# Kernel tuning notes

Measured on AMD Instinct MI355X. Metric: run time of the kernel, lower is better.

Reference implementation:

```python
import jax, jax.numpy as jnp
import numpy as np

N = 4096
D = 256
GW_EPSILON = 0.05
GW_MAX_ITER = 5
SINKHORN_MAX_ITER = 20
GAMMA = 1.0
LOG_EPS = 1e-10


def _sinkhorn(M, p, q, eps, n_iters):
    """Entropic OT: returns transport plan for cost M with marginals p, q."""
    K = jnp.exp(-M / eps)  # [n, n] Gibbs kernel

    def body(i, uv):
        u, v = uv
        u = p / (K @ v)
        v = q / (K.T @ u)
        return (u, v)

    u0 = jnp.ones_like(p)
    v0 = jnp.ones_like(q)
    u, v = jax.lax.fori_loop(0, n_iters, body, (u0, v0))
    return u[:, None] * K * v[None, :]  # diag(u) K diag(v)


def _entropic_gw(C1, C2, p, q, eps, gw_iters, sink_iters):
    """Entropic Gromov-Wasserstein with square_loss (POT-style fixed point)."""
    # square_loss decomposition: f1(a)=a^2, f2(b)=b^2, h1(a)=a, h2(b)=2b
    constC = (C1 ** 2 @ p)[:, None] + (C2 ** 2 @ q)[None, :]  # [n, n]
    hC1 = C1
    hC2 = 2.0 * C2
    T = jnp.outer(p, q)  # init plan

    def gw_body(i, T):
        tens = constC - hC1 @ (T @ hC2.T)  # gradient of GW objective
        return _sinkhorn(tens, p, q, eps, sink_iters)

    return jax.lax.fori_loop(0, gw_iters, gw_body, T)


def setup_inputs() -> dict:
    key = jax.random.key(0)
    k1, k2 = jax.random.split(key)
    features_1 = jax.random.normal(k1, (N, D), dtype=jnp.float32)
    features_2 = jax.random.normal(k2, (N, D), dtype=jnp.float32)
    return {"features_1": features_1, "features_2": features_2}


def reference(features_1, features_2):
    out_1 = features_1 / jnp.linalg.norm(features_1, axis=1, keepdims=True)
    out_2 = features_2 / jnp.linalg.norm(features_2, axis=1, keepdims=True)
    daa = 1.0 - out_1 @ out_1.T  # cosine-distance Gram, [n, n]
    dbb = 1.0 - out_2 @ out_2.T
    daa = daa / jnp.max(daa)
    dbb = dbb / jnp.max(dbb)
    n = daa.shape[0]
    p = jnp.full((n,), 1.0 / n, dtype=daa.dtype)
    q = jnp.full((n,), 1.0 / n, dtype=dbb.dtype)
    gw = _entropic_gw(daa, dbb, p, q, GW_EPSILON, GW_MAX_ITER, SINKHORN_MAX_ITER)
    loss = -jnp.sum(jnp.log(jnp.diag(gw) + LOG_EPS))
    return loss * GAMMA
```

## Files before the change

kernel.cpp:

```cpp
#include <hip/hip_runtime.h>

#define N4K 4096
#define DFEAT 256
constexpr float P_UNIF = 1.0f / 4096.0f;

typedef __attribute__((ext_vector_type(8))) short bf16x8;
typedef __attribute__((ext_vector_type(4))) float f32x4;

__device__ __forceinline__ float bfl(unsigned u) { return __uint_as_float(u << 16); }
__device__ __forceinline__ float bfh(unsigned u) { return __uint_as_float(u & 0xffff0000u); }
__device__ __forceinline__ unsigned short f2bf(float f) {
  unsigned u = __float_as_uint(f);
  u += 0x7fffu + ((u >> 16) & 1u);
  return (unsigned short)(u >> 16);
}
__device__ __forceinline__ unsigned char f2fp8(float v) {
  v = fminf(v, 448.0f);
  if (v < 0.015625f) return (unsigned char)__float2uint_rn(v * 512.0f);
  unsigned u = __float_as_uint(v);
  u += 0x7FFFFu + ((u >> 20) & 1u);
  return (unsigned char)(((u >> 20) & 0x7FF) - 960);
}
__device__ __forceinline__ void load_lds16(const void* g, void* l) {
  __builtin_amdgcn_global_load_lds(
      (const __attribute__((address_space(1))) void*)g,
      (__attribute__((address_space(3))) void*)l, 16, 0, 0);
}

#if __has_builtin(__builtin_amdgcn_cvt_pk_f32_fp8)
#define FP8_HW 1
#else
#define FP8_HW 0
#endif

__global__ void k_normalize(const float* __restrict__ in, unsigned short* __restrict__ out) {
  const int wv = threadIdx.x >> 6, lane = threadIdx.x & 63;
  const int row = blockIdx.x * 4 + wv;
  const float4 v = ((const float4*)(in + (size_t)row * DFEAT))[lane];
  float ss = v.x * v.x + v.y * v.y + v.z * v.z + v.w * v.w;
#pragma unroll
  for (int off = 32; off; off >>= 1) ss += __shfl_xor(ss, off);
  const float inv = rsqrtf(ss);
  unsigned a = (unsigned)f2bf(v.x * inv) | ((unsigned)f2bf(v.y * inv) << 16);
  unsigned b = (unsigned)f2bf(v.z * inv) | ((unsigned)f2bf(v.w * inv) << 16);
  ((uint2*)(out + (size_t)row * DFEAT))[lane] = make_uint2(a, b);
}

__global__ void k_transpose(const unsigned short* __restrict__ in,
                            unsigned short* __restrict__ out, int R, int C) {
  __shared__ unsigned short t[64][65];
  const int tid = threadIdx.x;
  const int tx = tid & 63, ty = tid >> 6;
  const int c0 = blockIdx.x * 64, r0 = blockIdx.y * 64;
#pragma unroll
  for (int k = 0; k < 16; k++) {
    const int r = ty * 16 + k;
    t[r][tx] = in[(size_t)(r0 + r) * C + c0 + tx];
  }
  __syncthreads();
#pragma unroll
  for (int k = 0; k < 16; k++) {
    const int r = ty * 16 + k;
    out[(size_t)(c0 + r) * R + r0 + tx] = t[tx][r];
  }
}

__global__ void k_zerof(float* __restrict__ p, int n) {
  const int i = blockIdx.x * 256 + threadIdx.x;
  if (i < n) p[i] = 0.0f;
}

__global__ __launch_bounds__(256) void k_gemm_bt(
    const unsigned short* __restrict__ A, const unsigned short* __restrict__ B,
    int ld, int kChunk, unsigned short* __restrict__ out, float* __restrict__ outf,
    int ldo, int mode, const float* __restrict__ ctE,
    const float* __restrict__ dm1, const float* __restrict__ dm2,
    float* __restrict__ psum, float* __restrict__ psq, float* __restrict__ dmx,
    unsigned char* __restrict__ K8, const float* __restrict__ shiftp)
{
  __shared__ __align__(16) unsigned char SMEM[16384];
  __shared__ float cs[128], cq[128];
  __shared__ float wmx[4];
  unsigned short* Als = (unsigned short*)SMEM;
  unsigned short* Bls = (unsigned short*)(SMEM + 8192);
  const int tid = threadIdx.x;
  const int w = tid >> 6, lane = tid & 63;
  const int wr = w >> 1, wc = w & 1;
  const int mbase = blockIdx.y * 128, nbase = blockIdx.x * 128;
  const int kBase = blockIdx.z * kChunk;

  if (mode == 4 && tid < 128) { cs[tid] = 0.f; cq[tid] = 0.f; }

  const f32x4 fz = {0.f, 0.f, 0.f, 0.f};
  f32x4 acc[4][4];
#pragma unroll
  for (int m = 0; m < 4; m++)
#pragma unroll
    for (int n = 0; n < 4; n++) acc[m][n] = fz;

  const int sRow = lane >> 2;
  const int sCol = (lane & 3) * 8;
  const unsigned short* gA = A + (size_t)(mbase + w * 32 + sRow) * ld + sCol;
  const unsigned short* gB = B + (size_t)(nbase + w * 32 + sRow) * ld + sCol;
  unsigned short* lA0 = &Als[(w * 2 + 0) * 512];
  unsigned short* lA1 = &Als[(w * 2 + 1) * 512];
  unsigned short* lB0 = &Bls[(w * 2 + 0) * 512];
  unsigned short* lB1 = &Bls[(w * 2 + 1) * 512];

  const int rA = lane & 15, kg = (lane >> 4) * 8;

  for (int k0 = kBase; k0 < kBase + kChunk; k0 += 32) {
    __syncthreads();
    load_lds16(gA + k0, lA0);
    load_lds16(gA + (size_t)16 * ld + k0, lA1);
    load_lds16(gB + k0, lB0);
    load_lds16(gB + (size_t)16 * ld + k0, lB1);
    __syncthreads();
    bf16x8 a[4], b[4];
#pragma unroll
    for (int m = 0; m < 4; m++)
      a[m] = *(const bf16x8*)&Als[(wr * 64 + m * 16 + rA) * 32 + kg];
#pragma unroll
    for (int n = 0; n < 4; n++)
      b[n] = *(const bf16x8*)&Bls[(wc * 64 + n * 16 + rA) * 32 + kg];
#pragma unroll
    for (int m = 0; m < 4; m++)
#pragma unroll
      for (int n = 0; n < 4; n++)
        acc[m][n] = __builtin_amdgcn_mfma_f32_16x16x32_bf16(a[m], b[n], acc[m][n], 0, 0, 0);
  }

  if (mode == 4) {
    float mx = -2.0f;
#pragma unroll
    for (int n = 0; n < 4; n++) {
      float sv = 0.f, sq2 = 0.f;
#pragma unroll
      for (int m = 0; m < 4; m++)
#pragma unroll
        for (int r = 0; r < 4; r++) {
          const float val = acc[m][n][r];
          sv += val; sq2 += val * val;
          mx = fmaxf(mx, -val);
        }
      const int lcol = wc * 64 + n * 16 + (lane & 15);
      atomicAdd(&cs[lcol], sv);
      atomicAdd(&cq[lcol], sq2);
    }
#pragma unroll
    for (int off = 32; off; off >>= 1) mx = fmaxf(mx, __shfl_xor(mx, off));
    if (lane == 0) wmx[w] = mx;
    __syncthreads();
    if (tid == 0)
      atomicMax((int*)dmx, __float_as_int(fmaxf(fmaxf(wmx[0], wmx[1]), fmaxf(wmx[2], wmx[3]))));
    if (tid < 128) {
      atomicAdd(&psum[nbase + tid], cs[tid]);
      atomicAdd(&psq[nbase + tid], cq[tid]);
    }
    return;
  }

  const int lrow16 = (lane >> 4) * 4;
  if (mode == 3) {
    float* ef = (float*)SMEM;
    for (int m = 0; m < 4; m++) {
      __syncthreads();
#pragma unroll
      for (int n = 0; n < 4; n++) {
        const int col = wc * 64 + n * 16 + (lane & 15);
#pragma unroll
        for (int r = 0; r < 4; r++)
          ef[(wr * 16 + lrow16 + r) * 128 + col] = acc[m][n][r];
      }
      __syncthreads();
#pragma unroll
      for (int h = 0; h < 4; h++) {
        const int t = tid + h * 256;
        const int cr = t >> 5, cc = (t & 31) * 4;
        const int grow = mbase + (cr >> 4) * 64 + m * 16 + (cr & 15);
        *(uint4*)&outf[((size_t)blockIdx.z * (gridDim.y * 128) + grow) * ldo + nbase + cc]
            = *(uint4*)&ef[cr * 128 + cc];
      }
    }
  } else if (mode == 2) {
    const float sArg = 40.0f / ((1.0f + *dm1) * (1.0f + *dm2));
    const float sh = *shiftp;
    unsigned short* eb = (unsigned short*)SMEM;
    unsigned char* eb8 = (unsigned char*)(SMEM + 8704);
    for (int m = 0; m < 4; m++) {
      __syncthreads();
#pragma unroll
      for (int n = 0; n < 4; n++) {
        const int col = wc * 64 + n * 16 + (lane & 15);
        const float cv = ctE[nbase + col] + sh;
#pragma unroll
        for (int r = 0; r < 4; r++) {
          const float val = __expf(fmaf(sArg, acc[m][n][r], -cv));
          eb[(wr * 16 + lrow16 + r) * 136 + col] = f2bf(val);
          eb8[(wr * 16 + lrow16 + r) * 144 + col] = f2fp8(val);
        }
      }
      __syncthreads();
#pragma unroll
      for (int h = 0; h < 2; h++) {
        const int t = tid + h * 256;
        const int cr = t >> 4, cc = (t & 15) * 8;
        const int grow = mbase + (cr >> 4) * 64 + m * 16 + (cr & 15);
        *(uint4*)&out[(size_t)grow * ldo + nbase + cc] = *(uint4*)&eb[cr * 136 + cc];
      }
      {
        const int cr = tid >> 3, cc = (tid & 7) * 16;
        const int grow = mbase + (cr >> 4) * 64 + m * 16 + (cr & 15);
        *(uint4*)&K8[(size_t)grow * N4K + nbase + cc] = *(uint4*)&eb8[cr * 144 + cc];
      }
    }
  } else {
    unsigned short* eb = (unsigned short*)SMEM;
    for (int m = 0; m < 4; m++) {
      __syncthreads();
#pragma unroll
      for (int n = 0; n < 4; n++) {
        const int col = wc * 64 + n * 16 + (lane & 15);
#pragma unroll
        for (int r = 0; r < 4; r++)
          eb[(wr * 16 + lrow16 + r) * 136 + col] = f2bf(acc[m][n][r]);
      }
      __syncthreads();
#pragma unroll
      for (int h = 0; h < 2; h++) {
        const int t = tid + h * 256;
        const int cr = t >> 4, cc = (t & 15) * 8;
        const int grow = mbase + (cr >> 4) * 64 + m * 16 + (cr & 15);
        *(uint4*)&out[(size_t)grow * ldo + nbase + cc] = *(uint4*)&eb[cr * 136 + cc];
      }
    }
  }
}

__global__ void k_ctfinal(const float* __restrict__ psum, const float* __restrict__ psq,
                          const float* __restrict__ dm1p, const float* __restrict__ dm2p,
                          float* __restrict__ ctE, float* __restrict__ ctsum) {
  __shared__ float red[256];
  const int tid = threadIdx.x;
  const int j = blockIdx.x * 256 + tid;
  const float g2 = psum[j] * (1.0f / N4K);
  const float s2 = psq[j] * (1.0f / N4K);
  const float m1 = 1.0f + *dm1p, m2 = 1.0f + *dm2p;
  const float v = ((1.0f - 2.0f * g2 + s2) / (m2 * m2) + (2.0f / (m1 * m2)) * g2) * 20.0f;
  ctE[j] = v;
  red[tid] = v;
  __syncthreads();
  for (int st = 128; st > 0; st >>= 1) {
    if (tid < st) red[tid] += red[tid + st];
    __syncthreads();
  }
  if (tid == 0) atomicAdd(ctsum, red[0]);
}

__global__ void k_yt0(const unsigned short* __restrict__ X2t, unsigned short* __restrict__ Yt,
                      float* __restrict__ x2sum) {
  __shared__ float red[256];
  const int d = blockIdx.x, t = threadIdx.x;
  const unsigned short* row = X2t + (size_t)d * N4K;
  const uint4 q = *(const uint4*)&row[t * 16];
  const uint4 q2 = *(const uint4*)&row[t * 16 + 8];
  float s = bfl(q.x) + bfh(q.x) + bfl(q.y) + bfh(q.y) + bfl(q.z) + bfh(q.z)
          + bfl(q.w) + bfh(q.w) + bfl(q2.x) + bfh(q2.x) + bfl(q2.y) + bfh(q2.y)
          + bfl(q2.z) + bfh(q2.z) + bfl(q2.w) + bfh(q2.w);
  red[t] = s;
  __syncthreads();
  for (int st = 128; st > 0; st >>= 1) {
    if (t < st) red[t] += red[t + st];
    __syncthreads();
  }
  if (t == 0) x2sum[d] = red[0];
  const unsigned short pv = f2bf(red[0] * (P_UNIF * P_UNIF));
  const unsigned pk = (unsigned)pv | ((unsigned)pv << 16);
  uint4* dst = (uint4*)(Yt + (size_t)d * N4K);
  dst[t] = make_uint4(pk, pk, pk, pk);
  dst[t + 256] = make_uint4(pk, pk, pk, pk);
}

__global__ void k_x2v(const unsigned short* __restrict__ X2t, const float* __restrict__ v,
                      unsigned short* __restrict__ X2vt) {
  const int d = blockIdx.x, t = threadIdx.x;
  const int i0 = t * 16;
  const unsigned short* src = X2t + (size_t)d * N4K + i0;
  unsigned short* dst = X2vt + (size_t)d * N4K + i0;
  const uint4 a = *(const uint4*)src;
  const uint4 b = *(const uint4*)(src + 8);
  const float4 v0 = *(const float4*)&v[i0];
  const float4 v1 = *(const float4*)&v[i0 + 4];
  const float4 v2 = *(const float4*)&v[i0 + 8];
  const float4 v3 = *(const float4*)&v[i0 + 12];
  unsigned r0 = (unsigned)f2bf(bfl(a.x) * v0.x) | ((unsigned)f2bf(bfh(a.x) * v0.y) << 16);
  unsigned r1 = (unsigned)f2bf(bfl(a.y) * v0.z) | ((unsigned)f2bf(bfh(a.y) * v0.w) << 16);
  unsigned r2 = (unsigned)f2bf(bfl(a.z) * v1.x) | ((unsigned)f2bf(bfh(a.z) * v1.y) << 16);
  unsigned r3 = (unsigned)f2bf(bfl(a.w) * v1.z) | ((unsigned)f2bf(bfh(a.w) * v1.w) << 16);
  unsigned r4 = (unsigned)f2bf(bfl(b.x) * v2.x) | ((unsigned)f2bf(bfh(b.x) * v2.y) << 16);
  unsigned r5 = (unsigned)f2bf(bfl(b.y) * v2.z) | ((unsigned)f2bf(bfh(b.y) * v2.w) << 16);
  unsigned r6 = (unsigned)f2bf(bfl(b.z) * v3.x) | ((unsigned)f2bf(bfh(b.z) * v3.y) << 16);
  unsigned r7 = (unsigned)f2bf(bfl(b.w) * v3.z) | ((unsigned)f2bf(bfh(b.w) * v3.w) << 16);
  *(uint4*)dst = make_uint4(r0, r1, r2, r3);
  *(uint4*)(dst + 8) = make_uint4(r4, r5, r6, r7);
}

__global__ void k_redY(const float* __restrict__ Yp, const float* __restrict__ u,
                       unsigned short* __restrict__ Yt) {
  __shared__ float t[64][65];
  const int tid = threadIdx.x;
  const int tx = tid & 63, ty = tid >> 6;
  const int r0 = blockIdx.x * 64, c0 = blockIdx.y * 64;
#pragma unroll
  for (int k = 0; k < 16; k++) {
    const int r = ty * 16 + k;
    const size_t off = (size_t)(r0 + r) * 256 + c0 + tx;
    float s = 0.f;
#pragma unroll
    for (int z = 0; z < 4; z++) s += Yp[(size_t)z * (N4K * 256) + off];
    t[r][tx] = s;
  }
  __syncthreads();
  const float uu = u[r0 + tx];
#pragma unroll
  for (int k = 0; k < 16; k++) {
    const int r = ty * 16 + k;
    Yt[(size_t)(c0 + r) * N4K + r0 + tx] = f2bf(t[tx][r] * uu);
  }
}

__global__ void k_redPT(const float* __restrict__ Pp, unsigned short* __restrict__ PTb) {
  const int idx = blockIdx.x * 256 + threadIdx.x;
  float s = 0.f;
#pragma unroll
  for (int z = 0; z < 16; z++) s += Pp[z * 65536 + idx];
  PTb[idx] = f2bf(s);
}

__global__ void k_zcol(const unsigned short* __restrict__ Zb, float* __restrict__ zpart) {
  const int c = threadIdx.x;
  const int r0 = blockIdx.x * 64;
  float s = 0.f;
  for (int r = 0; r < 64; r++)
    s += bfl((unsigned)Zb[(size_t)(r0 + r) * 256 + c]);
  zpart[blockIdx.x * 256 + c] = s;
}

__global__ void k_shift(const float* __restrict__ zpart, const float* __restrict__ x2sum,
                        const float* __restrict__ ctsum, const float* __restrict__ dm1,
                        const float* __restrict__ dm2, float* __restrict__ shift) {
  __shared__ float red[256];
  const int c = threadIdx.x;
  float zc = 0.f;
#pragma unroll
  for (int b = 0; b < 64; b++) zc += zpart[b * 256 + c];
  red[c] = zc * x2sum[c];
  __syncthreads();
  for (int st = 128; st > 0; st >>= 1) {
    if (c < st) red[c] += red[c + st];
    __syncthreads();
  }
  if (c == 0) {
    const float meanacc = red[0] * (1.0f / (16777216.0f));
    const float sArg = 40.0f / ((1.0f + *dm1) * (1.0f + *dm2));
    shift[0] = sArg * meanacc - ctsum[0] * (1.0f / N4K);
  }
}

__global__ __launch_bounds__(512) void k_sink8(
    const unsigned char* __restrict__ K8, const float* __restrict__ vin,
    float* __restrict__ u, float* __restrict__ partials, int first, int last)
{
  __shared__ float vs[N4K];
  __shared__ float lut[256];
  __shared__ float us[16];
  const int tid = threadIdx.x;
  if (tid < 256) {
    const int e = (tid >> 3) & 15, m = tid & 7;
    lut[tid] = e ? ldexpf((float)(8 + m), e - 10) : ldexpf((float)m, -9);
  }
  if (first) {
    for (int i = tid; i < N4K; i += 512) vs[i] = 1.0f;
  } else {
    float4* vl = (float4*)vs;
    const float4* vg = (const float4*)vin;
    vl[tid] = vg[tid];
    vl[tid + 512] = vg[tid + 512];
  }
  __syncthreads();
  const int wv = tid >> 6, lane = tid & 63;
  const int row0 = blockIdx.x * 16;

#if FP8_HW
#define DEC4(W, J, ACC) { \
    auto _lo = __builtin_amdgcn_cvt_pk_f32_fp8((int)(W), false); \
    auto _hi = __builtin_amdgcn_cvt_pk_f32_fp8((int)(W), true);  \
    ACC += _lo[0] * vs[(J)] + _lo[1] * vs[(J) + 1] + _hi[0] * vs[(J) + 2] + _hi[1] * vs[(J) + 3]; }
#else
#define DEC4(W, J, ACC) { \
    ACC += lut[(W) & 255] * vs[(J)] + lut[((W) >> 8) & 255] * vs[(J) + 1] \
         + lut[((W) >> 16) & 255] * vs[(J) + 2] + lut[(W) >> 24] * vs[(J) + 3]; }
#endif

  {
    const uint4* rA = (const uint4*)(K8 + (size_t)(row0 + wv * 2) * N4K);
    const uint4* rB = (const uint4*)(K8 + (size_t)(row0 + wv * 2 + 1) * N4K);
    float accA = 0.f, accB = 0.f;
#pragma unroll
    for (int p = 0; p < 4; p++) {
      const int j0 = p * 1024 + lane * 16;
      const uint4 qa = rA[p * 64 + lane];
      const uint4 qb = rB[p * 64 + lane];
      DEC4(qa.x, j0, accA); DEC4(qa.y, j0 + 4, accA);
      DEC4(qa.z, j0 + 8, accA); DEC4(qa.w, j0 + 12, accA);
      DEC4(qb.x, j0, accB); DEC4(qb.y, j0 + 4, accB);
      DEC4(qb.z, j0 + 8, accB); DEC4(qb.w, j0 + 12, accB);
    }
#pragma unroll
    for (int off = 32; off; off >>= 1) {
      accA += __shfl_xor(accA, off);
      accB += __shfl_xor(accB, off);
    }
    if (lane == 0) {
      us[wv * 2] = P_UNIF / accA;
      us[wv * 2 + 1] = P_UNIF / accB;
    }
  }
  __syncthreads();
  float uu[16];
#pragma unroll
  for (int r = 0; r < 16; r++) uu[r] = us[r];
  {
    const int c0 = tid * 8;
    const unsigned char* base = K8 + (size_t)row0 * N4K + c0;
    float a0 = 0, a1 = 0, a2 = 0, a3 = 0, a4 = 0, a5 = 0, a6 = 0, a7 = 0;
#pragma unroll
    for (int r = 0; r < 16; r++) {
      const uint2 q = *(const uint2*)(base + (size_t)r * N4K);
      const float ur = uu[r];
#if FP8_HW
      auto l0 = __builtin_amdgcn_cvt_pk_f32_fp8((int)q.x, false);
      auto h0 = __builtin_amdgcn_cvt_pk_f32_fp8((int)q.x, true);
      auto l1 = __builtin_amdgcn_cvt_pk_f32_fp8((int)q.y, false);
      auto h1 = __builtin_amdgcn_cvt_pk_f32_fp8((int)q.y, true);
      a0 += ur * l0[0]; a1 += ur * l0[1]; a2 += ur * h0[0]; a3 += ur * h0[1];
      a4 += ur * l1[0]; a5 += ur * l1[1]; a6 += ur * h1[0]; a7 += ur * h1[1];
#else
      a0 += ur * lut[q.x & 255]; a1 += ur * lut[(q.x >> 8) & 255];
      a2 += ur * lut[(q.x >> 16) & 255]; a3 += ur * lut[q.x >> 24];
      a4 += ur * lut[q.y & 255]; a5 += ur * lut[(q.y >> 8) & 255];
      a6 += ur * lut[(q.y >> 16) & 255]; a7 += ur * lut[q.y >> 24];
#endif
    }
    float* pp = partials + (size_t)blockIdx.x * N4K + c0;
    *(float4*)pp = make_float4(a0, a1, a2, a3);
    *(float4*)(pp + 4) = make_float4(a4, a5, a6, a7);
  }
  if (last && tid < 16) u[row0 + tid] = us[tid];
}

__global__ void k_sinkfin(const float* __restrict__ partials, float* __restrict__ v) {
  __shared__ float red[8][32];
  const int tid = threadIdx.x;
  const int c = (blockIdx.x << 5) + (tid & 31);
  const int s = tid >> 5;
  float acc = 0.f;
  const float* p = partials + (size_t)s * 32 * N4K + c;
#pragma unroll 8
  for (int b = 0; b < 32; b++) acc += p[(size_t)b * N4K];
  red[s][tid & 31] = acc;
  __syncthreads();
  if (s == 0) {
    float t = red[0][tid] + red[1][tid] + red[2][tid] + red[3][tid]
            + red[4][tid] + red[5][tid] + red[6][tid] + red[7][tid];
    v[c] = P_UNIF / t;
  }
}

__global__ void k_loss(const unsigned short* __restrict__ K, const float* __restrict__ u,
                       const float* __restrict__ v, float* __restrict__ out) {
  const int tid = threadIdx.x;
  float acc = 0.f;
  for (int i = tid; i < N4K; i += 256) {
    const float d = u[i] * bfl((unsigned)K[(size_t)i * (N4K + 1)]) * v[i];
    acc += logf(d + 1e-10f);
  }
  __shared__ float red[256];
  red[tid] = acc;
  __syncthreads();
  for (int st = 128; st > 0; st >>= 1) {
    if (tid < st) red[tid] += red[tid + st];
    __syncthreads();
  }
  if (tid == 0) out[0] = -red[0];
}

extern "C" void kernel_launch(void* const* d_in, const int* in_sizes, int n_in,
                              void* d_out, int out_size, void* d_ws, size_t ws_size,
                              hipStream_t stream) {
  const float* f1 = (const float*)d_in[0];
  const float* f2 = (const float*)d_in[1];
  float* out = (float*)d_out;

  char* w = (char*)d_ws;
  const size_t NN = (size_t)N4K * N4K;
  unsigned short* X1 = (unsigned short*)w;   w += (size_t)N4K * DFEAT * 2;
  unsigned short* X2 = (unsigned short*)w;   w += (size_t)N4K * DFEAT * 2;
  unsigned short* X1t = (unsigned short*)w;  w += (size_t)N4K * DFEAT * 2;
  unsigned short* X2t = (unsigned short*)w;  w += (size_t)N4K * DFEAT * 2;
  unsigned short* X2vt = (unsigned short*)w; w += (size_t)N4K * DFEAT * 2;
  unsigned short* Zb = (unsigned short*)w;   w += (size_t)N4K * DFEAT * 2;
  unsigned short* Yt = (unsigned short*)w;   w += (size_t)N4K * DFEAT * 2;
  unsigned short* PTb = (unsigned short*)w;  w += (size_t)DFEAT * DFEAT * 2;
  unsigned short* KA = (unsigned short*)w;   w += NN * 2;
  unsigned short* KB = (unsigned short*)w;   w += NN * 2;
  unsigned char* K8 = (unsigned char*)w;     w += NN;
  float* Yp = (float*)w;    w += (size_t)4 * N4K * DFEAT * 4;
  float* Pp = (float*)w;    w += (size_t)16 * DFEAT * DFEAT * 4;
  float* spart = (float*)w; w += (size_t)256 * N4K * 4;
  float* zpart = (float*)w; w += (size_t)64 * 256 * 4;
  float* stats = (float*)w; w += (size_t)16704 * 4;
  float* uvec = (float*)w;  w += N4K * 4;
  float* vvec = (float*)w;  w += N4K * 4;
  float* ctE = (float*)w;   w += N4K * 4;
  float* x2sum = (float*)w; w += 256 * 4;

  float* psum2 = stats;
  float* psq2 = stats + 4096;
  float* psumD = stats + 8192;
  float* psqD = stats + 12288;
  float* dmax1 = stats + 16384;
  float* dmax2 = stats + 16385;
  float* ctsum = stats + 16386;
  float* shiftv = stats + 16387;

  const dim3 b256(256);

  k_normalize<<<1024, b256, 0, stream>>>(f1, X1);
  k_normalize<<<1024, b256, 0, stream>>>(f2, X2);
  k_transpose<<<dim3(4, 64), b256, 0, stream>>>(X1, X1t, N4K, DFEAT);
  k_transpose<<<dim3(4, 64), b256, 0, stream>>>(X2, X2t, N4K, DFEAT);
  k_zerof<<<66, b256, 0, stream>>>(stats, 16704);

  k_gemm_bt<<<dim3(32, 32, 1), b256, 0, stream>>>(X1, X1, DFEAT, DFEAT, nullptr, nullptr,
                                                  0, 4, nullptr, nullptr, nullptr,
                                                  psumD, psqD, dmax1, nullptr, nullptr);
  k_gemm_bt<<<dim3(32, 32, 1), b256, 0, stream>>>(X2, X2, DFEAT, DFEAT, nullptr, nullptr,
                                                  0, 4, nullptr, nullptr, nullptr,
                                                  psum2, psq2, dmax2, nullptr, nullptr);
  k_ctfinal<<<16, b256, 0, stream>>>(psum2, psq2, dmax1, dmax2, ctE, ctsum);

  unsigned short* Kprev = nullptr;
  for (int it = 0; it < 5; it++) {
    if (it == 0) {
      k_yt0<<<256, b256, 0, stream>>>(X2t, Yt, x2sum);
    } else {
      k_x2v<<<256, b256, 0, stream>>>(X2t, vvec, X2vt);
      k_gemm_bt<<<dim3(2, 32, 4), b256, 0, stream>>>(Kprev, X2vt, N4K, 1024, nullptr, Yp,
                                                     DFEAT, 3, nullptr, nullptr, nullptr,
                                                     nullptr, nullptr, nullptr, nullptr, nullptr);
      k_redY<<<dim3(64, 4), b256, 0, stream>>>(Yp, uvec, Yt);
    }
    k_gemm_bt<<<dim3(2, 2, 16), b256, 0, stream>>>(Yt, X1t, N4K, 256, nullptr, Pp,
                                                   DFEAT, 3, nullptr, nullptr, nullptr,
                                                   nullptr, nullptr, nullptr, nullptr, nullptr);
    k_redPT<<<256, b256, 0, stream>>>(Pp, PTb);
    k_gemm_bt<<<dim3(2, 32, 1), b256, 0, stream>>>(X1, PTb, DFEAT, DFEAT, Zb, nullptr,
                                                   DFEAT, 0, nullptr, nullptr, nullptr,
                                                   nullptr, nullptr, nullptr, nullptr, nullptr);
    k_zcol<<<64, b256, 0, stream>>>(Zb, zpart);
    k_shift<<<1, b256, 0, stream>>>(zpart, x2sum, ctsum, dmax1, dmax2, shiftv);
    unsigned short* Knew = (Kprev == KA) ? KB : KA;
    k_gemm_bt<<<dim3(32, 32, 1), b256, 0, stream>>>(Zb, X2, DFEAT, DFEAT, Knew, nullptr,
                                                    N4K, 2, ctE, dmax1, dmax2,
                                                    nullptr, nullptr, nullptr, K8, shiftv);
    for (int s = 0; s < 20; s++) {
      k_sink8<<<256, dim3(512), 0, stream>>>(K8, vvec, uvec, spart,
                                             s == 0 ? 1 : 0, s == 19 ? 1 : 0);
      k_sinkfin<<<128, b256, 0, stream>>>(spart, vvec);
    }
    Kprev = Knew;
  }
  k_loss<<<1, b256, 0, stream>>>(Kprev, uvec, vvec, out);
}
```

Measured before the change: 1.561 ms.

## Use FP8 Gibbs kernel for T@X2 GEMM and drop bf16 K copy

The bf16 copy of the Gibbs kernel is no longer written. The K·(v∘X2) GEMM now reads the FP8 kernel through a new FP8 MFMA path, with v∘X2 quantized to scaled signed FP8; the scale is undone in redY. The shift computation is rewritten algebraically as PTb·x1sum, using a precomputed column sum of X1, which removes the Zb column-reduction kernel. This cuts 32 MB of bf16 writes per outer iteration and halves GEMM input bandwidth, at the cost of reduced precision in the transport-plan product and in the loss diagonal.

```diff
diff --git a/kernel.cpp b/kernel.cpp
--- a/kernel.cpp
+++ b/kernel.cpp
@@ -14,12 +14,20 @@
   u += 0x7fffu + ((u >> 16) & 1u);
   return (unsigned short)(u >> 16);
 }
-__device__ __forceinline__ unsigned char f2fp8(float v) {
+__device__ __forceinline__ unsigned f2fp8(float v) {
   v = fminf(v, 448.0f);
-  if (v < 0.015625f) return (unsigned char)__float2uint_rn(v * 512.0f);
+  if (v < 0.015625f) return __float2uint_rn(v * 512.0f);
   unsigned u = __float_as_uint(v);
   u += 0x7FFFFu + ((u >> 20) & 1u);
-  return (unsigned char)(((u >> 20) & 0x7FF) - 960);
+  return ((u >> 20) & 0x7FF) - 960;
+}
+__device__ __forceinline__ unsigned f2fp8s(float v) {
+  const unsigned s = (__float_as_uint(v) >> 24) & 0x80u;
+  return s | f2fp8(fabsf(v));
+}
+__device__ __forceinline__ float fp8dec(unsigned b) {
+  const int e = (b >> 3) & 15, m = b & 7;
+  return e ? ldexpf((float)(8 + m), e - 10) : ldexpf((float)m, -9);
 }
 __device__ __forceinline__ void load_lds16(const void* g, void* l) {
   __builtin_amdgcn_global_load_lds(
@@ -68,6 +76,24 @@
 __global__ void k_zerof(float* __restrict__ p, int n) {
   const int i = blockIdx.x * 256 + threadIdx.x;
   if (i < n) p[i] = 0.0f;
+}
+
+__global__ void k_rsum(const unsigned short* __restrict__ Xt, float* __restrict__ s256) {
+  __shared__ float red[256];
+  const int d = blockIdx.x, t = threadIdx.x;
+  const unsigned short* row = Xt + (size_t)d * N4K;
+  const uint4 q = *(const uint4*)&row[t * 16];
+  const uint4 q2 = *(const uint4*)&row[t * 16 + 8];
+  float s = bfl(q.x) + bfh(q.x) + bfl(q.y) + bfh(q.y) + bfl(q.z) + bfh(q.z)
+          + bfl(q.w) + bfh(q.w) + bfl(q2.x) + bfh(q2.x) + bfl(q2.y) + bfh(q2.y)
+          + bfl(q2.z) + bfh(q2.z) + bfl(q2.w) + bfh(q2.w);
+  red[t] = s;
+  __syncthreads();
+  for (int st = 128; st > 0; st >>= 1) {
+    if (t < st) red[t] += red[t + st];
+    __syncthreads();
+  }
+  if (t == 0) s256[d] = red[0];
 }
 
 __global__ __launch_bounds__(256) void k_gemm_bt(
@@ -81,8 +107,6 @@
   __shared__ __align__(16) unsigned char SMEM[16384];
   __shared__ float cs[128], cq[128];
   __shared__ float wmx[4];
-  unsigned short* Als = (unsigned short*)SMEM;
-  unsigned short* Bls = (unsigned short*)(SMEM + 8192);
   const int tid = threadIdx.x;
   const int w = tid >> 6, lane = tid & 63;
   const int wr = w >> 1, wc = w & 1;
@@ -98,36 +122,68 @@
 #pragma unroll
     for (int n = 0; n < 4; n++) acc[m][n] = fz;
 
-  const int sRow = lane >> 2;
-  const int sCol = (lane & 3) * 8;
-  const unsigned short* gA = A + (size_t)(mbase + w * 32 + sRow) * ld + sCol;
-  const unsigned short* gB = B + (size_t)(nbase + w * 32 + sRow) * ld + sCol;
-  unsigned short* lA0 = &Als[(w * 2 + 0) * 512];
-  unsigned short* lA1 = &Als[(w * 2 + 1) * 512];
-  unsigned short* lB0 = &Bls[(w * 2 + 0) * 512];
-  unsigned short* lB1 = &Bls[(w * 2 + 1) * 512];
-
-  const int rA = lane & 15, kg = (lane >> 4) * 8;
-
-  for (int k0 = kBase; k0 < kBase + kChunk; k0 += 32) {
-    __syncthreads();
-    load_lds16(gA + k0, lA0);
-    load_lds16(gA + (size_t)16 * ld + k0, lA1);
-    load_lds16(gB + k0, lB0);
-    load_lds16(gB + (size_t)16 * ld + k0, lB1);
-    __syncthreads();
-    bf16x8 a[4], b[4];
-#pragma unroll
-    for (int m = 0; m < 4; m++)
-      a[m] = *(const bf16x8*)&Als[(wr * 64 + m * 16 + rA) * 32 + kg];
-#pragma unroll
-    for (int n = 0; n < 4; n++)
-      b[n] = *(const bf16x8*)&Bls[(wc * 64 + n * 16 + rA) * 32 + kg];
-#pragma unroll
-    for (int m = 0; m < 4; m++)
+  const int rA = lane & 15;
+
+  if (mode == 5) {
+    const unsigned char* A8 = (const unsigned char*)A;
+    const unsigned char* B8 = (const unsigned char*)B;
+    unsigned char* As8 = SMEM;
+    unsigned char* Bs8 = SMEM + 4096;
+    const unsigned char* gA8 = A8 + (size_t)(mbase + w * 32 + (lane >> 1)) * ld + (lane & 1) * 16;
+    const unsigned char* gB8 = B8 + (size_t)(nbase + w * 32 + (lane >> 1)) * ld + (lane & 1) * 16;
+    unsigned char* lA8 = As8 + w * 1024;
+    unsigned char* lB8 = Bs8 + w * 1024;
+    const int kg8 = (lane >> 4) * 8;
+    for (int k0 = kBase; k0 < kBase + kChunk; k0 += 32) {
+      __syncthreads();
+      load_lds16(gA8 + k0, lA8);
+      load_lds16(gB8 + k0, lB8);
+      __syncthreads();
+      long a8[4], b8[4];
+#pragma unroll
+      for (int m = 0; m < 4; m++)
+        a8[m] = *(const long*)&As8[(wr * 64 + m * 16 + rA) * 32 + kg8];
 #pragma unroll
       for (int n = 0; n < 4; n++)
-        acc[m][n] = __builtin_amdgcn_mfma_f32_16x16x32_bf16(a[m], b[n], acc[m][n], 0, 0, 0);
+        b8[n] = *(const long*)&Bs8[(wc * 64 + n * 16 + rA) * 32 + kg8];
+#pragma unroll
+      for (int m = 0; m < 4; m++)
+#pragma unroll
+        for (int n = 0; n < 4; n++)
+          acc[m][n] = __builtin_amdgcn_mfma_f32_16x16x32_fp8_fp8(a8[m], b8[n], acc[m][n], 0, 0, 0);
+    }
+  } else {
+    unsigned short* Als = (unsigned short*)SMEM;
+    unsigned short* Bls = (unsigned short*)(SMEM + 8192);
+    const int sRow = lane >> 2;
+    const int sCol = (lane & 3) * 8;
+    const unsigned short* gA = A + (size_t)(mbase + w * 32 + sRow) * ld + sCol;
+    const unsigned short* gB = B + (size_t)(nbase + w * 32 + sRow) * ld + sCol;
+    unsigned short* lA0 = &Als[(w * 2 + 0) * 512];
+    unsigned short* lA1 = &Als[(w * 2 + 1) * 512];
+    unsigned short* lB0 = &Bls[(w * 2 + 0) * 512];
+    unsigned short* lB1 = &Bls[(w * 2 + 1) * 512];
+    const int kg = (lane >> 4) * 8;
+    for (int k0 = kBase; k0 < kBase + kChunk; k0 += 32) {
+      __syncthreads();
+      load_lds16(gA + k0, lA0);
+      load_lds16(gA + (size_t)16 * ld + k0, lA1);
+      load_lds16(gB + k0, lB0);
+      load_lds16(gB + (size_t)16 * ld + k0, lB1);
+      __syncthreads();
+      bf16x8 a[4], b[4];
+#pragma unroll
+      for (int m = 0; m < 4; m++)
+        a[m] = *(const bf16x8*)&Als[(wr * 64 + m * 16 + rA) * 32 + kg];
+#pragma unroll
+      for (int n = 0; n < 4; n++)
+        b[n] = *(const bf16x8*)&Bls[(wc * 64 + n * 16 + rA) * 32 + kg];
+#pragma unroll
+      for (int m = 0; m < 4; m++)
+#pragma unroll
+        for (int n = 0; n < 4; n++)
+          acc[m][n] = __builtin_amdgcn_mfma_f32_16x16x32_bf16(a[m], b[n], acc[m][n], 0, 0, 0);
+    }
   }
 
   if (mode == 4) {
@@ -161,7 +217,7 @@
   }
 
   const int lrow16 = (lane >> 4) * 4;
-  if (mode == 3) {
+  if (mode == 3 || mode == 5) {
     float* ef = (float*)SMEM;
     for (int m = 0; m < 4; m++) {
       __syncthreads();
@@ -185,8 +241,7 @@
   } else if (mode == 2) {
     const float sArg = 40.0f / ((1.0f + *dm1) * (1.0f + *dm2));
     const float sh = *shiftp;
-    unsigned short* eb = (unsigned short*)SMEM;
-    unsigned char* eb8 = (unsigned char*)(SMEM + 8704);
+    unsigned char* eb8 = SMEM;
     for (int m = 0; m < 4; m++) {
       __syncthreads();
 #pragma unroll
@@ -196,18 +251,10 @@
 #pragma unroll
         for (int r = 0; r < 4; r++) {
           const float val = __expf(fmaf(sArg, acc[m][n][r], -cv));
-          eb[(wr * 16 + lrow16 + r) * 136 + col] = f2bf(val);
-          eb8[(wr * 16 + lrow16 + r) * 144 + col] = f2fp8(val);
+          eb8[(wr * 16 + lrow16 + r) * 144 + col] = (unsigned char)f2fp8(val);
         }
       }
       __syncthreads();
-#pragma unroll
-      for (int h = 0; h < 2; h++) {
-        const int t = tid + h * 256;
-        const int cr = t >> 4, cc = (t & 15) * 8;
-        const int grow = mbase + (cr >> 4) * 64 + m * 16 + (cr & 15);
-        *(uint4*)&out[(size_t)grow * ldo + nbase + cc] = *(uint4*)&eb[cr * 136 + cc];
-      }
       {
         const int cr = tid >> 3, cc = (tid & 7) * 16;
         const int grow = mbase + (cr >> 4) * 64 + m * 16 + (cr & 15);
@@ -281,28 +328,27 @@
   dst[t + 256] = make_uint4(pk, pk, pk, pk);
 }
 
-__global__ void k_x2v(const unsigned short* __restrict__ X2t, const float* __restrict__ v,
-                      unsigned short* __restrict__ X2vt) {
+__global__ void k_x2v8(const unsigned short* __restrict__ X2t, const float* __restrict__ v,
+                       unsigned char* __restrict__ X2vt8) {
   const int d = blockIdx.x, t = threadIdx.x;
   const int i0 = t * 16;
   const unsigned short* src = X2t + (size_t)d * N4K + i0;
-  unsigned short* dst = X2vt + (size_t)d * N4K + i0;
   const uint4 a = *(const uint4*)src;
   const uint4 b = *(const uint4*)(src + 8);
   const float4 v0 = *(const float4*)&v[i0];
   const float4 v1 = *(const float4*)&v[i0 + 4];
   const float4 v2 = *(const float4*)&v[i0 + 8];
   const float4 v3 = *(const float4*)&v[i0 + 12];
-  unsigned r0 = (unsigned)f2bf(bfl(a.x) * v0.x) | ((unsigned)f2bf(bfh(a.x) * v0.y) << 16);
-  unsigned r1 = (unsigned)f2bf(bfl(a.y) * v0.z) | ((unsigned)f2bf(bfh(a.y) * v0.w) << 16);
-  unsigned r2 = (unsigned)f2bf(bfl(a.z) * v1.x) | ((unsigned)f2bf(bfh(a.z) * v1.y) << 16);
-  unsigned r3 = (unsigned)f2bf(bfl(a.w) * v1.z) | ((unsigned)f2bf(bfh(a.w) * v1.w) << 16);
-  unsigned r4 = (unsigned)f2bf(bfl(b.x) * v2.x) | ((unsigned)f2bf(bfh(b.x) * v2.y) << 16);
-  unsigned r5 = (unsigned)f2bf(bfl(b.y) * v2.z) | ((unsigned)f2bf(bfh(b.y) * v2.w) << 16);
-  unsigned r6 = (unsigned)f2bf(bfl(b.z) * v3.x) | ((unsigned)f2bf(bfh(b.z) * v3.y) << 16);
-  unsigned r7 = (unsigned)f2bf(bfl(b.w) * v3.z) | ((unsigned)f2bf(bfh(b.w) * v3.w) << 16);
-  *(uint4*)dst = make_uint4(r0, r1, r2, r3);
-  *(uint4*)(dst + 8) = make_uint4(r4, r5, r6, r7);
+  const float C = 4096.0f;
+  unsigned w0 = f2fp8s(bfl(a.x) * v0.x * C) | (f2fp8s(bfh(a.x) * v0.y * C) << 8)
+              | (f2fp8s(bfl(a.y) * v0.z * C) << 16) | (f2fp8s(bfh(a.y) * v0.w * C) << 24);
+  unsigned w1 = f2fp8s(bfl(a.z) * v1.x * C) | (f2fp8s(bfh(a.z) * v1.y * C) << 8)
+              | (f2fp8s(bfl(a.w) * v1.z * C) << 16) | (f2fp8s(bfh(a.w) * v1.w * C) << 24);
+  unsigned w2 = f2fp8s(bfl(b.x) * v2.x * C) | (f2fp8s(bfh(b.x) * v2.y * C) << 8)
+              | (f2fp8s(bfl(b.y) * v2.z * C) << 16) | (f2fp8s(bfh(b.y) * v2.w * C) << 24);
+  unsigned w3 = f2fp8s(bfl(b.z) * v3.x * C) | (f2fp8s(bfh(b.z) * v3.y * C) << 8)
+              | (f2fp8s(bfl(b.w) * v3.z * C) << 16) | (f2fp8s(bfh(b.w) * v3.w * C) << 24);
+  *(uint4*)(X2vt8 + (size_t)d * N4K + i0) = make_uint4(w0, w1, w2, w3);
 }
 
 __global__ void k_redY(const float* __restrict__ Yp, const float* __restrict__ u,
@@ -321,7 +367,7 @@
     t[r][tx] = s;
   }
   __syncthreads();
-  const float uu = u[r0 + tx];
+  const float uu = u[r0 + tx] * P_UNIF;
 #pragma unroll
   for (int k = 0; k < 16; k++) {
     const int r = ty * 16 + k;
@@ -337,31 +383,23 @@
   PTb[idx] = f2bf(s);
 }
 
-__global__ void k_zcol(const unsigned short* __restrict__ Zb, float* __restrict__ zpart) {
-  const int c = threadIdx.x;
-  const int r0 = blockIdx.x * 64;
-  float s = 0.f;
-  for (int r = 0; r < 64; r++)
-    s += bfl((unsigned)Zb[(size_t)(r0 + r) * 256 + c]);
-  zpart[blockIdx.x * 256 + c] = s;
-}
-
-__global__ void k_shift(const float* __restrict__ zpart, const float* __restrict__ x2sum,
-                        const float* __restrict__ ctsum, const float* __restrict__ dm1,
-                        const float* __restrict__ dm2, float* __restrict__ shift) {
+__global__ void k_shift2(const unsigned short* __restrict__ PTb, const float* __restrict__ x1sum,
+                         const float* __restrict__ x2sum, const float* __restrict__ ctsum,
+                         const float* __restrict__ dm1, const float* __restrict__ dm2,
+                         float* __restrict__ shift) {
   __shared__ float red[256];
-  const int c = threadIdx.x;
+  const int d = threadIdx.x;
   float zc = 0.f;
-#pragma unroll
-  for (int b = 0; b < 64; b++) zc += zpart[b * 256 + c];
-  red[c] = zc * x2sum[c];
+  const unsigned short* row = PTb + d * 256;
+  for (int e = 0; e < 256; e++) zc += bfl((unsigned)row[e]) * x1sum[e];
+  red[d] = zc * x2sum[d];
   __syncthreads();
   for (int st = 128; st > 0; st >>= 1) {
-    if (c < st) red[c] += red[c + st];
+    if (d < st) red[d] += red[d + st];
     __syncthreads();
   }
-  if (c == 0) {
-    const float meanacc = red[0] * (1.0f / (16777216.0f));
+  if (d == 0) {
+    const float meanacc = red[0] * (1.0f / 16777216.0f);
     const float sArg = 40.0f / ((1.0f + *dm1) * (1.0f + *dm2));
     shift[0] = sArg * meanacc - ctsum[0] * (1.0f / N4K);
   }
@@ -375,10 +413,7 @@
   __shared__ float lut[256];
   __shared__ float us[16];
   const int tid = threadIdx.x;
-  if (tid < 256) {
-    const int e = (tid >> 3) & 15, m = tid & 7;
-    lut[tid] = e ? ldexpf((float)(8 + m), e - 10) : ldexpf((float)m, -9);
-  }
+  if (tid < 256) lut[tid] = fp8dec(tid);
   if (first) {
     for (int i = tid; i < N4K; i += 512) vs[i] = 1.0f;
   } else {
@@ -477,12 +512,12 @@
   }
 }
 
-__global__ void k_loss(const unsigned short* __restrict__ K, const float* __restrict__ u,
+__global__ void k_loss(const unsigned char* __restrict__ K8, const float* __restrict__ u,
                        const float* __restrict__ v, float* __restrict__ out) {
   const int tid = threadIdx.x;
   float acc = 0.f;
   for (int i = tid; i < N4K; i += 256) {
-    const float d = u[i] * bfl((unsigned)K[(size_t)i * (N4K + 1)]) * v[i];
+    const float d = u[i] * fp8dec(K8[(size_t)i * (N4K + 1)]) * v[i];
     acc += logf(d + 1e-10f);
   }
   __shared__ float red[256];
@@ -508,22 +543,20 @@
   unsigned short* X2 = (unsigned short*)w;   w += (size_t)N4K * DFEAT * 2;
   unsigned short* X1t = (unsigned short*)w;  w += (size_t)N4K * DFEAT * 2;
   unsigned short* X2t = (unsigned short*)w;  w += (size_t)N4K * DFEAT * 2;
-  unsigned short* X2vt = (unsigned short*)w; w += (size_t)N4K * DFEAT * 2;
+  unsigned char* X2vt8 = (unsigned char*)w;  w += (size_t)N4K * DFEAT;
   unsigned short* Zb = (unsigned short*)w;   w += (size_t)N4K * DFEAT * 2;
   unsigned short* Yt = (unsigned short*)w;   w += (size_t)N4K * DFEAT * 2;
   unsigned short* PTb = (unsigned short*)w;  w += (size_t)DFEAT * DFEAT * 2;
-  unsigned short* KA = (unsigned short*)w;   w += NN * 2;
-  unsigned short* KB = (unsigned short*)w;   w += NN * 2;
   unsigned char* K8 = (unsigned char*)w;     w += NN;
   float* Yp = (float*)w;    w += (size_t)4 * N4K * DFEAT * 4;
   float* Pp = (float*)w;    w += (size_t)16 * DFEAT * DFEAT * 4;
   float* spart = (float*)w; w += (size_t)256 * N4K * 4;
-  float* zpart = (float*)w; w += (size_t)64 * 256 * 4;
   float* stats = (float*)w; w += (size_t)16704 * 4;
   float* uvec = (float*)w;  w += N4K * 4;
   float* vvec = (float*)w;  w += N4K * 4;
   float* ctE = (float*)w;   w += N4K * 4;
   float* x2sum = (float*)w; w += 256 * 4;
+  float* x1sum = (float*)w; w += 256 * 4;
 
   float* psum2 = stats;
   float* psq2 = stats + 4096;
@@ -540,6 +573,7 @@
   k_normalize<<<1024, b256, 0, stream>>>(f2, X2);
   k_transpose<<<dim3(4, 64), b256, 0, stream>>>(X1, X1t, N4K, DFEAT);
   k_transpose<<<dim3(4, 64), b256, 0, stream>>>(X2, X2t, N4K, DFEAT);
+  k_rsum<<<256, b256, 0, stream>>>(X1t, x1sum);
   k_zerof<<<66, b256, 0, stream>>>(stats, 16704);
 
   k_gemm_bt<<<dim3(32, 32, 1), b256, 0, stream>>>(X1, X1, DFEAT, DFEAT, nullptr, nullptr,
@@ -550,14 +584,15 @@
                                                   psum2, psq2, dmax2, nullptr, nullptr);
   k_ctfinal<<<16, b256, 0, stream>>>(psum2, psq2, dmax1, dmax2, ctE, ctsum);
 
-  unsigned short* Kprev = nullptr;
   for (int it = 0; it < 5; it++) {
     if (it == 0) {
       k_yt0<<<256, b256, 0, stream>>>(X2t, Yt, x2sum);
     } else {
-      k_x2v<<<256, b256, 0, stream>>>(X2t, vvec, X2vt);
-      k_gemm_bt<<<dim3(2, 32, 4), b256, 0, stream>>>(Kprev, X2vt, N4K, 1024, nullptr, Yp,
-                                                     DFEAT, 3, nullptr, nullptr, nullptr,
+      k_x2v8<<<256, b256, 0, stream>>>(X2t, vvec, X2vt8);
+      k_gemm_bt<<<dim3(2, 32, 4), b256, 0, stream>>>((const unsigned short*)K8,
+                                                     (const unsigned short*)X2vt8,
+                                                     N4K, 1024, nullptr, Yp,
+                                                     DFEAT, 5, nullptr, nullptr, nullptr,
                                                      nullptr, nullptr, nullptr, nullptr, nullptr);
       k_redY<<<dim3(64, 4), b256, 0, stream>>>(Yp, uvec, Yt);
     }
@@ -568,10 +603,8 @@
     k_gemm_bt<<<dim3(2, 32, 1), b256, 0, stream>>>(X1, PTb, DFEAT, DFEAT, Zb, nullptr,
                                                    DFEAT, 0, nullptr, nullptr, nullptr,
                                                    nullptr, nullptr, nullptr, nullptr, nullptr);
-    k_zcol<<<64, b256, 0, stream>>>(Zb, zpart);
-    k_shift<<<1, b256, 0, stream>>>(zpart, x2sum, ctsum, dmax1, dmax2, shiftv);
-    unsigned short* Knew = (Kprev == KA) ? KB : KA;
-    k_gemm_bt<<<dim3(32, 32, 1), b256, 0, stream>>>(Zb, X2, DFEAT, DFEAT, Knew, nullptr,
+    k_shift2<<<1, b256, 0, stream>>>(PTb, x1sum, x2sum, ctsum, dmax1, dmax2, shiftv);
+    k_gemm_bt<<<dim3(32, 32, 1), b256, 0, stream>>>(Zb, X2, DFEAT, DFEAT, nullptr, nullptr,
                                                     N4K, 2, ctE, dmax1, dmax2,
                                                     nullptr, nullptr, nullptr, K8, shiftv);
     for (int s = 0; s < 20; s++) {
@@ -579,7 +612,6 @@
                                              s == 0 ? 1 : 0, s == 19 ? 1 : 0);
       k_sinkfin<<<128, b256, 0, stream>>>(spart, vvec);
     }
-    Kprev = Knew;
-  }
-  k_loss<<<1, b256, 0, stream>>>(Kprev, uvec, vvec, out);
-}
+  }
+  k_loss<<<1, b256, 0, stream>>>(K8, uvec, vvec, out);
+}
```

After: 1.551 ms. No clear change (-0.6%).
